# Optimization experiments

Measured on AMD Instinct MI355X. Metric: run time of the kernel, lower is better.

The kernel has to match this reference:

```python
import jax, jax.numpy as jnp
import numpy as np

VOCAB, D_MODEL, HEADS, PAD_ID = 32000, 512, 8, 0
D_K = D_MODEL // HEADS
EPS = 1e-5


def pos_encoding(T, d):
    pos = jnp.arange(T, dtype=jnp.float32)[:, None]              # [T,1]
    freqs = 1.0 / (10000.0 ** (jnp.arange(0, d, 2, dtype=jnp.float32) / d))
    ang = pos * freqs                                            # [T,d/2]
    pe = jnp.zeros((T, d), dtype=jnp.float32)
    pe = pe.at[:, 0::2].set(jnp.sin(ang)).at[:, 1::2].set(jnp.cos(ang))
    return pe


def layer_norm(x, g, b):
    mu = jnp.mean(x, axis=-1, keepdims=True)
    var = jnp.var(x, axis=-1, keepdims=True)
    return (x - mu) * jax.lax.rsqrt(var + EPS) * g + b


def setup_inputs() -> dict:
    key = jax.random.key(0)
    ks = jax.random.split(key, 12)
    B, T = 4, 2048
    s = 0.02
    inp = {
        "tokens": jax.random.randint(ks[0], (B, T), 0, VOCAB),
        "emb": jax.random.normal(ks[1], (VOCAB, D_MODEL), jnp.float32) * s,
        "wq": jax.random.normal(ks[2], (D_MODEL, D_MODEL), jnp.float32) * s,
        "bq": jnp.zeros((D_MODEL,), jnp.float32),
        "wk": jax.random.normal(ks[3], (D_MODEL, D_MODEL), jnp.float32) * s,
        "bk": jnp.zeros((D_MODEL,), jnp.float32),
        "wv": jax.random.normal(ks[4], (D_MODEL, D_MODEL), jnp.float32) * s,
        "bv": jnp.zeros((D_MODEL,), jnp.float32),
        "wo": jax.random.normal(ks[5], (D_MODEL, D_MODEL), jnp.float32) * s,
        "bo": jnp.zeros((D_MODEL,), jnp.float32),
        "w1": jax.random.normal(ks[6], (D_MODEL, 2 * D_MODEL), jnp.float32) * s,
        "b1": jnp.zeros((2 * D_MODEL,), jnp.float32),
        "w2": jax.random.normal(ks[7], (2 * D_MODEL, D_MODEL), jnp.float32) * s,
        "b2": jnp.zeros((D_MODEL,), jnp.float32),
        "ln1_g": jnp.ones((D_MODEL,), jnp.float32),
        "ln1_b": jnp.zeros((D_MODEL,), jnp.float32),
        "ln2_g": jnp.ones((D_MODEL,), jnp.float32),
        "ln2_b": jnp.zeros((D_MODEL,), jnp.float32),
    }
    return inp


def reference(tokens, emb, wq, bq, wk, bk, wv, bv, wo, bo,
              w1, b1, w2, b2, ln1_g, ln1_b, ln2_g, ln2_b):
    B, T = tokens.shape
    x = emb[tokens] * jnp.sqrt(jnp.float32(D_MODEL))             # [B,T,D]
    x = x + pos_encoding(T, D_MODEL)[None]                       # add PE
    q = (x @ wq + bq).reshape(B, T, HEADS, D_K)
    k = (x @ wk + bk).reshape(B, T, HEADS, D_K)
    v = (x @ wv + bv).reshape(B, T, HEADS, D_K)
    scores = jnp.einsum("bqhd,bkhd->bhqk", q, k) / jnp.sqrt(jnp.float32(D_K))
    key_pad_mask = tokens == PAD_ID                              # [B,T]
    neg = jnp.finfo(scores.dtype).min
    scores = jnp.where(key_pad_mask[:, None, None, :], neg, scores)
    attn = jax.nn.softmax(scores, axis=-1)                       # [B,H,T,T]
    av = jnp.einsum("bhqk,bkhd->bqhd", attn, v).reshape(B, T, D_MODEL)
    av = av @ wo + bo
    h = layer_norm(av + x, ln1_g, ln1_b)
    ff = jax.nn.relu(h @ w1 + b1) @ w2 + b2
    out = layer_norm(h + ff, ln2_g, ln2_b)
    return out, key_pad_mask
```

## Files before the change

kernel.cpp:

```cpp
#include <hip/hip_runtime.h>
#include <hip/hip_bf16.h>
#include <math.h>

#define D_MODEL 512
#define HEADS   8
#define D_K     64
#define T_SEQ   2048
#define B_SZ    4
#define NROWS   (B_SZ * T_SEQ)
#define KVB     64
#define KSPLIT  2
#define KHALF   (T_SEQ / KSPLIT)

#define BN 128
#define BKG 64

typedef __attribute__((ext_vector_type(8))) short short8;
typedef __attribute__((ext_vector_type(4))) float f32x4;
typedef __attribute__((ext_vector_type(4))) ushort bf16x4;
typedef __attribute__((ext_vector_type(4))) unsigned int u32x4;

typedef __attribute__((address_space(1))) const unsigned int as1_uint;
typedef __attribute__((address_space(3))) unsigned int as3_uint;

__device__ __forceinline__ ushort f2bf(float f) {
    union { float f; unsigned u; } v; v.f = f;
    unsigned u = v.u;
    unsigned r = (u + 0x7FFFu + ((u >> 16) & 1u)) >> 16;
    return (ushort)r;
}
__device__ __forceinline__ float bf2f(ushort u) {
    union { unsigned u; float f; } v; v.u = ((unsigned)u) << 16;
    return v.f;
}
__device__ __forceinline__ unsigned pk_bf16(float lo, float hi) {
    unsigned r;
    asm("v_cvt_pk_bf16_f32 %0, %1, %2" : "=v"(r) : "v"(lo), "v"(hi));
    return r;
}

__global__ __launch_bounds__(256) void k_prep(
    const int* __restrict__ tokens, const float* __restrict__ emb,
    const float* __restrict__ wq, const float* __restrict__ wk,
    const float* __restrict__ wv, const float* __restrict__ wo,
    const float* __restrict__ w1, const float* __restrict__ w2,
    const float* __restrict__ bq, const float* __restrict__ bk,
    const float* __restrict__ bv,
    ushort* __restrict__ xb, float* __restrict__ mask_out,
    ushort* __restrict__ wqkvT, ushort* __restrict__ woT,
    ushort* __restrict__ w1T, ushort* __restrict__ w2T,
    float* __restrict__ bqkv, float qsc)
{
    __shared__ ushort tls[32][33];
    int bid = blockIdx.x, tid = threadIdx.x;
    if (bid < 4096) {
        int row = bid * 2 + (tid >> 7);
        int t   = row & (T_SEQ - 1);
        int tok = tokens[row];
        int t2  = tid & 127;
        if (t2 == 0) mask_out[row] = (tok == 0) ? 1.0f : 0.0f;
        const float* e = emb + (size_t)tok * D_MODEL;
#pragma unroll
        for (int i = 0; i < 4; ++i) {
            int d = t2 + 128 * i;
            float freq = exp2f(-(float)(d & ~1) * 0.025952563240330564f);
            float sn, cs;
            sincosf((float)t * freq, &sn, &cs);
            float x = e[d] * 22.627416997969522f + ((d & 1) ? cs : sn);
            xb[(size_t)row * D_MODEL + d] = f2bf(x);
        }
        return;
    }
    const float* src; ushort* dst; float scale = 1.0f; int K, N, bx, by;
    if (bid < 5120) {
        int b = bid - 4096; int z = b >> 8; int rem = b & 255;
        bx = rem & 15; by = rem >> 4; K = 512; N = 512;
        src = (z == 0) ? wq : (z == 1) ? wk : (z == 2) ? wv : wo;
        dst = (z < 3) ? wqkvT + (size_t)z * 512 * 512 : woT;
        scale = (z == 0) ? qsc : 1.0f;
    } else if (bid < 5632) {
        int b = bid - 5120; bx = b & 31; by = b >> 5; K = 512; N = 1024; src = w1; dst = w1T;
    } else if (bid < 6144) {
        int b = bid - 5632; bx = b & 15; by = b >> 4; K = 1024; N = 512; src = w2; dst = w2T;
    } else {
        int i = (bid - 6144) * 256 + tid;
        if (i < 512)       bqkv[i] = bq[i] * qsc;
        else if (i < 1024) bqkv[i] = bk[i - 512];
        else if (i < 1536) bqkv[i] = bv[i - 1024];
        return;
    }
    int tx = tid & 31, ty = tid >> 5;
    int n0 = bx * 32, k0 = by * 32;
#pragma unroll
    for (int i = 0; i < 4; ++i)
        tls[ty + i * 8][tx] = f2bf(src[(size_t)(k0 + ty + i * 8) * N + n0 + tx] * scale);
    __syncthreads();
#pragma unroll
    for (int i = 0; i < 4; ++i)
        dst[(size_t)(n0 + ty + i * 8) * K + k0 + tx] = tls[tx][ty + i * 8];
}

template<int MODE, bool RELU, int BMT>
__global__ __launch_bounds__(256) void k_gemm_lds(
    const ushort* __restrict__ A, const ushort* __restrict__ BT,
    const float* __restrict__ bias, void* __restrict__ C0,
    void* __restrict__ C1, void* __restrict__ C2,
    int M, int N, int K)
{
    constexpr int MR = BMT / 32;
    __shared__ __attribute__((aligned(16))) ushort As[2][BMT * BKG];
    __shared__ __attribute__((aligned(16))) ushort Bs[2][BN * BKG];

    const int tid = threadIdx.x;
    const int w = tid >> 6, l = tid & 63;
    const int lr = l & 15, lg = l >> 4;
    const int wr = w >> 1, wc = w & 1;

    int bx = blockIdx.x, by = blockIdx.y;
    {
        int nx = gridDim.x, ny = gridDim.y;
        if ((ny & 7) == 0) {
            int lin = bx + nx * by;
            int xcd = lin & 7, idx = lin >> 3;
            int per = ny >> 3;
            by = xcd * per + (idx % per);
            bx = idx / per;
        }
    }
    const int brow0 = by * BMT;
    const int bcol0 = bx * BN;
    const int swz = lr & 15 & 7;

    f32x4 acc[MR][4] = {};
    const int nks = K >> 6;

#define STAGE(buf, k0)                                                          \
    {                                                                           \
        _Pragma("unroll")                                                       \
        for (int i = 0; i < BMT / 32; ++i) {                                    \
            int gi = w * (BMT * 2) + i * 64 + l;                                \
            int row = gi >> 3, slot = gi & 7;                                   \
            int g = slot ^ (row & 7);                                           \
            __builtin_amdgcn_global_load_lds(                                   \
                (as1_uint*)(A + (size_t)(brow0 + row) * K + (k0) + g * 8),      \
                (as3_uint*)(&As[buf][gi * 8]), 16, 0, 0);                       \
        }                                                                       \
        _Pragma("unroll")                                                       \
        for (int i = 0; i < 4; ++i) {                                           \
            int gi = w * 256 + i * 64 + l;                                      \
            int row = gi >> 3, slot = gi & 7;                                   \
            int g = slot ^ (row & 7);                                           \
            __builtin_amdgcn_global_load_lds(                                   \
                (as1_uint*)(BT + (size_t)(bcol0 + row) * K + (k0) + g * 8),     \
                (as3_uint*)(&Bs[buf][gi * 8]), 16, 0, 0);                       \
        }                                                                       \
    }

    STAGE(0, 0);
    __syncthreads();

    int buf = 0;
    for (int ks = 0; ks < nks; ++ks) {
        if (ks + 1 < nks) STAGE(buf ^ 1, (ks + 1) * BKG);
#pragma unroll
        for (int kk = 0; kk < 2; ++kk) {
            short8 af[MR], bfr[4];
#pragma unroll
            for (int m = 0; m < MR; ++m) {
                int row = wr * (BMT / 2) + m * 16 + lr;
                int slot = (kk * 4 + lg) ^ swz;
                af[m] = *(const short8*)(&As[buf][row * 64 + slot * 8]);
            }
#pragma unroll
            for (int n = 0; n < 4; ++n) {
                int row = wc * 64 + n * 16 + lr;
                int slot = (kk * 4 + lg) ^ swz;
                bfr[n] = *(const short8*)(&Bs[buf][row * 64 + slot * 8]);
            }
#pragma unroll
            for (int m = 0; m < MR; ++m)
#pragma unroll
                for (int n = 0; n < 4; ++n)
                    acc[m][n] = __builtin_amdgcn_mfma_f32_16x16x32_bf16(af[m], bfr[n], acc[m][n], 0, 0, 0);
        }
        __syncthreads();
        buf ^= 1;
    }
#undef STAGE

#pragma unroll
    for (int n = 0; n < 4; ++n) {
        int col = bcol0 + wc * 64 + n * 16 + lr;
        float bv = bias[col];
#pragma unroll
        for (int m = 0; m < MR; ++m) {
            int row0 = brow0 + wr * (BMT / 2) + m * 16 + 4 * lg;
            if constexpr (MODE == 2) {
                int seg = col >> 9, lc = col & 511;
                if (seg == 2) {
                    bf16x4 pk;
#pragma unroll
                    for (int j = 0; j < 4; ++j) pk[j] = f2bf(acc[m][n][j] + bv);
                    *(bf16x4*)((ushort*)C2 + (size_t)lc * M + row0) = pk;
                } else {
                    ushort* dst = (seg == 0) ? (ushort*)C0 : (ushort*)C1;
#pragma unroll
                    for (int j = 0; j < 4; ++j)
                        dst[(size_t)(row0 + j) * 512 + lc] = f2bf(acc[m][n][j] + bv);
                }
            } else if constexpr (MODE == 0) {
#pragma unroll
                for (int j = 0; j < 4; ++j) {
                    float v = acc[m][n][j] + bv;
                    if (RELU) v = fmaxf(v, 0.0f);
                    ((ushort*)C0)[(size_t)(row0 + j) * N + col] = f2bf(v);
                }
            } else {
#pragma unroll
                for (int j = 0; j < 4; ++j)
                    ((float*)C0)[(size_t)(row0 + j) * N + col] = acc[m][n][j] + bv;
            }
        }
    }
}

__global__ __launch_bounds__(512, 4) void k_attn(
    const ushort* __restrict__ Q, const ushort* __restrict__ Kb,
    const ushort* __restrict__ Vt, const int* __restrict__ tokens,
    ushort* __restrict__ O0, ushort* __restrict__ O1,
    float* __restrict__ lp)
{
    __shared__ __attribute__((aligned(16))) ushort Kl[2][KVB * 64];
    __shared__ __attribute__((aligned(16))) ushort Vl[2][KVB * 64];
    __shared__ __attribute__((aligned(16))) ushort Mbh[KHALF];
    __shared__ int padf[KHALF / KVB];

    const int tid = threadIdx.x;
    const int w = tid >> 6, l = tid & 63;
    const int lr = l & 15, lg = l >> 4;
    const int swz = lr & 7;

    int lin = blockIdx.x + 8 * (blockIdx.y + 8 * blockIdx.z);
    int xcd = lin & 7, idx = lin >> 3;
    int qt  = idx & 7;
    int grp = xcd + 8 * (idx >> 3);
    int ks  = grp & 1;
    int h   = (grp >> 1) & 7;
    int b   = grp >> 4;

    const int q0  = qt * 256 + w * 32;
    const int kb0 = ks * KHALF;

    const int gi   = w * 64 + l;
    const int srow = gi >> 3;
    const int sg   = gi & 7;
    const int sgx  = sg ^ (srow & 7);
    const ushort* Ksrc = Kb + ((size_t)(b * T_SEQ + kb0) + srow) * D_MODEL + h * D_K + sgx * 8;
    const int kbase = 32 * (sg >> 2) + 8 * ((sg >> 1) & 1) + 4 * (sg & 1);
    const ushort* Vsrc = Vt + (size_t)(h * D_K + srow) * NROWS + b * T_SEQ + kb0 + kbase;
    const int vds = srow * 128 + sgx * 16;

#define KSTAGE(bufi, kt_)                                                       \
    __builtin_amdgcn_global_load_lds(                                           \
        (as1_uint*)(Ksrc + (size_t)(kt_) * KVB * D_MODEL),                      \
        (as3_uint*)(&Kl[bufi][gi * 8]), 16, 0, 0);

    const ushort* Qh = Q + (size_t)b * T_SEQ * D_MODEL + h * D_K;
    short8 aq[2][2];
#pragma unroll
    for (int qs = 0; qs < 2; ++qs)
#pragma unroll
        for (int c2 = 0; c2 < 2; ++c2)
            aq[qs][c2] = *(const short8*)(Qh + (size_t)(q0 + qs * 16 + lr) * D_MODEL
                                          + c2 * 32 + 8 * lg);

    short8 vones;
#pragma unroll
    for (int i = 0; i < 8; ++i) vones[i] = (short)0x3F80;

    const int* tk = tokens + b * T_SEQ + kb0;
#pragma unroll
    for (int it = 0; it < KHALF / 512; ++it) {
        int i = tid + it * 512;
        bool pad = (tk[i] == 0);
        Mbh[i] = pad ? (ushort)0xFF7F : (ushort)0;
        unsigned long long bal = __ballot(pad);
        if (l == 0) padf[it * 8 + w] = (bal != 0ull);
    }

    f32x4 acc[2][4] = {};
    f32x4 acc_l[2] = {};

    {
        bf16x4 va = *(const bf16x4*)(Vsrc);
        bf16x4 vb2 = *(const bf16x4*)(Vsrc + 16);
        KSTAGE(0, 0);
        u32x4 pk = { ((const unsigned*)&va)[0], ((const unsigned*)&va)[1],
                     ((const unsigned*)&vb2)[0], ((const unsigned*)&vb2)[1] };
        *(u32x4*)((char*)Vl[0] + vds) = pk;
    }
    __syncthreads();

    int buf = 0;
    const int NT = KHALF / KVB;
    for (int kt = 0; kt < NT; ++kt) {
        bf16x4 vna, vnb;
        bool more = (kt + 1 < NT);
        if (more) {
            KSTAGE(buf ^ 1, kt + 1);
            vna = *(const bf16x4*)(Vsrc + (kt + 1) * KVB);
            vnb = *(const bf16x4*)(Vsrc + (kt + 1) * KVB + 16);
        }

        const ushort* Kt = Kl[buf];
        const ushort* Vb = Vl[buf];
        bool havePad = padf[kt];

        unsigned dw[2][4][2];
#pragma unroll
        for (int kh = 0; kh < 2; ++kh) {
            short8 kf[2][2];
#pragma unroll
            for (int i = 0; i < 2; ++i)
#pragma unroll
                for (int c2 = 0; c2 < 2; ++c2)
                    kf[i][c2] = *(const short8*)((const char*)Kt
                                + ((2 * kh + i) * 16 + lr) * 128
                                + (((c2 * 4 + lg) ^ swz) * 16));
#pragma unroll
            for (int qs = 0; qs < 2; ++qs)
#pragma unroll
                for (int i = 0; i < 2; ++i) {
                    int kb = 2 * kh + i;
                    __builtin_amdgcn_s_setprio(1);
                    f32x4 sf = {};
                    sf = __builtin_amdgcn_mfma_f32_16x16x32_bf16(kf[i][0], aq[qs][0], sf, 0, 0, 0);
                    sf = __builtin_amdgcn_mfma_f32_16x16x32_bf16(kf[i][1], aq[qs][1], sf, 0, 0, 0);
                    __builtin_amdgcn_s_setprio(0);
                    if (havePad) {
                        bf16x4 m4 = *(const bf16x4*)(Mbh + kt * KVB + kb * 16 + 4 * lg);
#pragma unroll
                        for (int j = 0; j < 4; ++j) sf[j] += bf2f(m4[j]);
                    }
                    dw[qs][kb][0] = pk_bf16(exp2f(sf[0]), exp2f(sf[1]));
                    dw[qs][kb][1] = pk_bf16(exp2f(sf[2]), exp2f(sf[3]));
                }
        }

#pragma unroll
        for (int ch = 0; ch < 2; ++ch) {
            short8 vf[2][2];
#pragma unroll
            for (int i = 0; i < 2; ++i)
#pragma unroll
                for (int kk = 0; kk < 2; ++kk)
                    vf[i][kk] = *(const short8*)((const char*)Vb
                                + ((2 * ch + i) * 16 + lr) * 128
                                + (((kk * 4 + lg) ^ swz) * 16));
            __builtin_amdgcn_s_setprio(1);
#pragma unroll
            for (int qs = 0; qs < 2; ++qs) {
                u32x4 pw0 = { dw[qs][0][0], dw[qs][0][1], dw[qs][1][0], dw[qs][1][1] };
                u32x4 pw1 = { dw[qs][2][0], dw[qs][2][1], dw[qs][3][0], dw[qs][3][1] };
                short8 pa0 = __builtin_bit_cast(short8, pw0);
                short8 pa1 = __builtin_bit_cast(short8, pw1);
#pragma unroll
                for (int i = 0; i < 2; ++i) {
                    int c = 2 * ch + i;
                    acc[qs][c] = __builtin_amdgcn_mfma_f32_16x16x32_bf16(vf[i][0], pa0, acc[qs][c], 0, 0, 0);
                    acc[qs][c] = __builtin_amdgcn_mfma_f32_16x16x32_bf16(vf[i][1], pa1, acc[qs][c], 0, 0, 0);
                }
                if (ch == 0) {
                    acc_l[qs] = __builtin_amdgcn_mfma_f32_16x16x32_bf16(vones, pa0, acc_l[qs], 0, 0, 0);
                    acc_l[qs] = __builtin_amdgcn_mfma_f32_16x16x32_bf16(vones, pa1, acc_l[qs], 0, 0, 0);
                }
            }
            __builtin_amdgcn_s_setprio(0);
        }

        if (more) {
            u32x4 pk = { ((const unsigned*)&vna)[0], ((const unsigned*)&vna)[1],
                         ((const unsigned*)&vnb)[0], ((const unsigned*)&vnb)[1] };
            *(u32x4*)((char*)Vl[buf ^ 1] + vds) = pk;
        }
        __syncthreads();
        buf ^= 1;
    }
#undef KSTAGE

    ushort* Op = (ks == 0) ? O0 : O1;
#pragma unroll
    for (int qs = 0; qs < 2; ++qs) {
        ushort* orow = Op + (size_t)(b * T_SEQ + q0 + qs * 16 + lr) * D_MODEL + h * D_K;
#pragma unroll
        for (int c = 0; c < 4; ++c) {
            bf16x4 pk;
#pragma unroll
            for (int j = 0; j < 4; ++j) pk[j] = f2bf(acc[qs][c][j]);
            *(bf16x4*)(orow + c * 16 + 4 * lg) = pk;
        }
        if (l < 16)
            lp[(size_t)(ks * 8 + h) * NROWS + b * T_SEQ + q0 + qs * 16 + l] = acc_l[qs][0];
    }
}

__global__ __launch_bounds__(256) void k_comb(
    ushort* __restrict__ O0, const ushort* __restrict__ O1,
    const float* __restrict__ lp)
{
    int g = blockIdx.x * 256 + threadIdx.x;
    int row = g >> 6, seg = g & 63;
    int h = seg >> 3;
    size_t off = (size_t)row * D_MODEL + seg * 8;
    short8 a = *(const short8*)(O0 + off);
    short8 c = *(const short8*)(O1 + off);
    float l0 = lp[(size_t)h * NROWS + row];
    float l1 = lp[(size_t)(8 + h) * NROWS + row];
    float rl = 1.0f / (l0 + l1);
    short8 r;
#pragma unroll
    for (int i = 0; i < 8; ++i)
        r[i] = (short)f2bf((bf2f((ushort)a[i]) + bf2f((ushort)c[i])) * rl);
    *(short8*)(O0 + off) = r;
}

template<bool A_BF16, bool RES_BF16, bool OUT_F32>
__global__ __launch_bounds__(256) void k_ln(
    const void* __restrict__ A, const void* __restrict__ Res,
    const float* __restrict__ g, const float* __restrict__ bb,
    float* __restrict__ of, ushort* __restrict__ ob)
{
    int row = blockIdx.x * 4 + (threadIdx.x >> 6);
    int l = threadIdx.x & 63;
    float v[8];
    float s = 0.0f, ss = 0.0f;
#pragma unroll
    for (int i = 0; i < 2; ++i) {
        int d0 = i * 256 + l * 4;
        f32x4 va, vb;
        if (A_BF16) {
            bf16x4 t = *(const bf16x4*)((const ushort*)A + (size_t)row * D_MODEL + d0);
#pragma unroll
            for (int j = 0; j < 4; ++j) va[j] = bf2f(t[j]);
        } else {
            va = *(const f32x4*)((const float*)A + (size_t)row * D_MODEL + d0);
        }
        if (RES_BF16) {
            bf16x4 t = *(const bf16x4*)((const ushort*)Res + (size_t)row * D_MODEL + d0);
#pragma unroll
            for (int j = 0; j < 4; ++j) vb[j] = bf2f(t[j]);
        } else {
            vb = *(const f32x4*)((const float*)Res + (size_t)row * D_MODEL + d0);
        }
#pragma unroll
        for (int j = 0; j < 4; ++j) {
            float x = va[j] + vb[j];
            v[i * 4 + j] = x; s += x; ss += x * x;
        }
    }
#pragma unroll
    for (int d = 1; d < 64; d <<= 1) { s += __shfl_xor(s, d); ss += __shfl_xor(ss, d); }
    float mu  = s * (1.0f / 512.0f);
    float var = ss * (1.0f / 512.0f) - mu * mu;
    float rs  = rsqrtf(var + 1e-5f);
#pragma unroll
    for (int i = 0; i < 2; ++i)
#pragma unroll
        for (int j = 0; j < 4; ++j) {
            int d = i * 256 + l * 4 + j;
            float o = (v[i * 4 + j] - mu) * rs * g[d] + bb[d];
            if (OUT_F32) of[(size_t)row * D_MODEL + d] = o;
            else         ob[(size_t)row * D_MODEL + d] = f2bf(o);
        }
}

extern "C" void kernel_launch(void* const* d_in, const int* in_sizes, int n_in,
                              void* d_out, int out_size, void* d_ws, size_t ws_size,
                              hipStream_t stream)
{
    const int*   tokens = (const int*)  d_in[0];
    const float* emb    = (const float*)d_in[1];
    const float* wq     = (const float*)d_in[2];
    const float* bq     = (const float*)d_in[3];
    const float* wk     = (const float*)d_in[4];
    const float* bk     = (const float*)d_in[5];
    const float* wv     = (const float*)d_in[6];
    const float* bv     = (const float*)d_in[7];
    const float* wo     = (const float*)d_in[8];
    const float* bo     = (const float*)d_in[9];
    const float* w1     = (const float*)d_in[10];
    const float* b1     = (const float*)d_in[11];
    const float* w2     = (const float*)d_in[12];
    const float* b2     = (const float*)d_in[13];
    const float* ln1_g  = (const float*)d_in[14];
    const float* ln1_b  = (const float*)d_in[15];
    const float* ln2_g  = (const float*)d_in[16];
    const float* ln2_b  = (const float*)d_in[17];

    char* ws = (char*)d_ws;
    ushort* xb   = (ushort*)(ws + 0);
    ushort* Qb   = (ushort*)(ws + 8388608);
    ushort* Kbuf = (ushort*)(ws + 16777216);
    ushort* Vt   = (ushort*)(ws + 25165824);
    ushort* atb  = (ushort*)(ws + 33554432);
    ushort* AVb  = (ushort*)(ws + 41943040);
    ushort* wqkvT = (ushort*)(ws + 50331648);
    ushort* woT  = wqkvT + 1536 * 512;
    ushort* w1T  = woT + 262144;
    ushort* w2T  = w1T + 524288;
    float*  bqkv = (float*)(w2T + 524288);
    float*  lpart = bqkv + 2048;

    ushort* hb   = Qb;
    ushort* ff1b = Kbuf;
    ushort* ff2b = AVb;

    float* out_f    = (float*)d_out;
    float* mask_out = out_f + (size_t)NROWS * D_MODEL;

    const float QSC = 0.18033688011112042f;

    k_prep<<<6150, 256, 0, stream>>>(
        tokens, emb, wq, wk, wv, wo, w1, w2, bq, bk, bv,
        xb, mask_out, wqkvT, woT, w1T, w2T, bqkv, QSC);

    k_gemm_lds<2, false, 128><<<dim3(12, 64), 256, 0, stream>>>(
        xb, wqkvT, bqkv, Qb, Kbuf, Vt, NROWS, 1536, 512);

    k_attn<<<dim3(8, 8, 8), 512, 0, stream>>>(
        Qb, Kbuf, Vt, tokens, atb, AVb, lpart);
    k_comb<<<2048, 256, 0, stream>>>(atb, AVb, lpart);

    k_gemm_lds<0, false, 64><<<dim3(4, 128), 256, 0, stream>>>(
        atb, woT, bo, AVb, nullptr, nullptr, NROWS, 512, 512);

    k_ln<true, true, false><<<NROWS / 4, 256, 0, stream>>>(
        AVb, xb, ln1_g, ln1_b, nullptr, hb);

    k_gemm_lds<0, true, 64><<<dim3(8, 128), 256, 0, stream>>>(
        hb, w1T, b1, ff1b, nullptr, nullptr, NROWS, 1024, 512);
    k_gemm_lds<0, false, 64><<<dim3(4, 128), 256, 0, stream>>>(
        ff1b, w2T, b2, ff2b, nullptr, nullptr, NROWS, 512, 1024);

    k_ln<true, true, true><<<NROWS / 4, 256, 0, stream>>>(
        ff2b, hb, ln2_g, ln2_b, out_f, nullptr);
}
```

Before: 156.5 us.

## Fuse split-K attention combine into output-projection GEMM A-tile staging

Removes the separate combine kernel that merged the two key-split attention partial outputs. The Wo GEMM now loads both partial outputs per A tile, adds them, scales by a precomputed reciprocal normalizer from a tiny new kernel, and writes bf16 to LDS. This saves a full read-modify-write pass over the attention output, but the A path switches from async global-to-LDS DMA to register loads plus math. Buffers are also reassigned to avoid aliasing, and the attention key loop gets an unroll-2 pragma.

```diff
diff --git a/kernel.cpp b/kernel.cpp
--- a/kernel.cpp
+++ b/kernel.cpp
@@ -100,9 +100,17 @@
         dst[(size_t)(n0 + ty + i * 8) * K + k0 + tx] = tls[tx][ty + i * 8];
 }
 
-template<int MODE, bool RELU, int BMT>
+__global__ __launch_bounds__(256) void k_rl(const float* __restrict__ lp,
+                                            float* __restrict__ rl) {
+    int i = blockIdx.x * 256 + threadIdx.x;
+    rl[i] = 1.0f / (lp[i] + lp[8 * NROWS + i]);
+}
+
+template<int MODE, bool RELU, int BMT, bool COMBA>
 __global__ __launch_bounds__(256) void k_gemm_lds(
-    const ushort* __restrict__ A, const ushort* __restrict__ BT,
+    const ushort* __restrict__ A, const ushort* __restrict__ A2,
+    const float* __restrict__ rlb,
+    const ushort* __restrict__ BT,
     const float* __restrict__ bias, void* __restrict__ C0,
     void* __restrict__ C1, void* __restrict__ C2,
     int M, int N, int K)
@@ -129,12 +137,24 @@
     }
     const int brow0 = by * BMT;
     const int bcol0 = bx * BN;
-    const int swz = lr & 15 & 7;
+    const int swz = lr & 7;
 
     f32x4 acc[MR][4] = {};
     const int nks = K >> 6;
 
-#define STAGE(buf, k0)                                                          \
+#define STAGE_B(buf, k0)                                                        \
+    {                                                                           \
+        _Pragma("unroll")                                                       \
+        for (int i = 0; i < 4; ++i) {                                           \
+            int gi = w * 256 + i * 64 + l;                                      \
+            int row = gi >> 3, slot = gi & 7;                                   \
+            int g = slot ^ (row & 7);                                           \
+            __builtin_amdgcn_global_load_lds(                                   \
+                (as1_uint*)(BT + (size_t)(bcol0 + row) * K + (k0) + g * 8),     \
+                (as3_uint*)(&Bs[buf][gi * 8]), 16, 0, 0);                       \
+        }                                                                       \
+    }
+#define STAGE_A_DMA(buf, k0)                                                    \
     {                                                                           \
         _Pragma("unroll")                                                       \
         for (int i = 0; i < BMT / 32; ++i) {                                    \
@@ -145,15 +165,38 @@
                 (as1_uint*)(A + (size_t)(brow0 + row) * K + (k0) + g * 8),      \
                 (as3_uint*)(&As[buf][gi * 8]), 16, 0, 0);                       \
         }                                                                       \
+    }
+#define STAGE_A_COMB(buf, k0)                                                   \
+    {                                                                           \
+        int head = (k0) >> 6;                                                   \
         _Pragma("unroll")                                                       \
-        for (int i = 0; i < 4; ++i) {                                           \
-            int gi = w * 256 + i * 64 + l;                                      \
+        for (int i = 0; i < BMT / 32; ++i) {                                    \
+            int gi = w * (BMT * 2) + i * 64 + l;                                \
             int row = gi >> 3, slot = gi & 7;                                   \
             int g = slot ^ (row & 7);                                           \
-            __builtin_amdgcn_global_load_lds(                                   \
-                (as1_uint*)(BT + (size_t)(bcol0 + row) * K + (k0) + g * 8),     \
-                (as3_uint*)(&Bs[buf][gi * 8]), 16, 0, 0);                       \
+            size_t off = (size_t)(brow0 + row) * K + (k0) + g * 8;              \
+            bf16x4 a0 = *(const bf16x4*)(A + off);                              \
+            bf16x4 a1 = *(const bf16x4*)(A + off + 4);                          \
+            bf16x4 c0 = *(const bf16x4*)(A2 + off);                             \
+            bf16x4 c1 = *(const bf16x4*)(A2 + off + 4);                         \
+            float r = rlb[(size_t)head * NROWS + brow0 + row];                  \
+            u32x4 pk;                                                           \
+            pk[0] = pk_bf16((bf2f(a0[0]) + bf2f(c0[0])) * r,                    \
+                            (bf2f(a0[1]) + bf2f(c0[1])) * r);                   \
+            pk[1] = pk_bf16((bf2f(a0[2]) + bf2f(c0[2])) * r,                    \
+                            (bf2f(a0[3]) + bf2f(c0[3])) * r);                   \
+            pk[2] = pk_bf16((bf2f(a1[0]) + bf2f(c1[0])) * r,                    \
+                            (bf2f(a1[1]) + bf2f(c1[1])) * r);                   \
+            pk[3] = pk_bf16((bf2f(a1[2]) + bf2f(c1[2])) * r,                    \
+                            (bf2f(a1[3]) + bf2f(c1[3])) * r);                   \
+            *(u32x4*)(&As[buf][gi * 8]) = pk;                                   \
         }                                                                       \
+    }
+#define STAGE(buf, k0)                                                          \
+    {                                                                           \
+        if constexpr (COMBA) { STAGE_A_COMB(buf, k0); }                         \
+        else                 { STAGE_A_DMA(buf, k0); }                          \
+        STAGE_B(buf, k0);                                                       \
     }
 
     STAGE(0, 0);
@@ -187,6 +230,9 @@
         buf ^= 1;
     }
 #undef STAGE
+#undef STAGE_A_COMB
+#undef STAGE_A_DMA
+#undef STAGE_B
 
 #pragma unroll
     for (int n = 0; n < 4; ++n) {
@@ -303,6 +349,7 @@
 
     int buf = 0;
     const int NT = KHALF / KVB;
+#pragma unroll 2
     for (int kt = 0; kt < NT; ++kt) {
         bf16x4 vna, vnb;
         bool more = (kt + 1 < NT);
@@ -402,26 +449,6 @@
         if (l < 16)
             lp[(size_t)(ks * 8 + h) * NROWS + b * T_SEQ + q0 + qs * 16 + l] = acc_l[qs][0];
     }
-}
-
-__global__ __launch_bounds__(256) void k_comb(
-    ushort* __restrict__ O0, const ushort* __restrict__ O1,
-    const float* __restrict__ lp)
-{
-    int g = blockIdx.x * 256 + threadIdx.x;
-    int row = g >> 6, seg = g & 63;
-    int h = seg >> 3;
-    size_t off = (size_t)row * D_MODEL + seg * 8;
-    short8 a = *(const short8*)(O0 + off);
-    short8 c = *(const short8*)(O1 + off);
-    float l0 = lp[(size_t)h * NROWS + row];
-    float l1 = lp[(size_t)(8 + h) * NROWS + row];
-    float rl = 1.0f / (l0 + l1);
-    short8 r;
-#pragma unroll
-    for (int i = 0; i < 8; ++i)
-        r[i] = (short)f2bf((bf2f((ushort)a[i]) + bf2f((ushort)c[i])) * rl);
-    *(short8*)(O0 + off) = r;
 }
 
 template<bool A_BF16, bool RES_BF16, bool OUT_F32>
@@ -510,10 +537,14 @@
     ushort* w2T  = w1T + 524288;
     float*  bqkv = (float*)(w2T + 524288);
     float*  lpart = bqkv + 2048;
+    float*  rlbuf = lpart + 2 * 8 * NROWS;
+    float*  WOf   = (float*)(rlbuf + 8 * NROWS);
 
     ushort* hb   = Qb;
     ushort* ff1b = Kbuf;
     ushort* ff2b = AVb;
+    ushort* wob  = AVb;
+    (void)WOf;
 
     float* out_f    = (float*)d_out;
     float* mask_out = out_f + (size_t)NROWS * D_MODEL;
@@ -524,24 +555,24 @@
         tokens, emb, wq, wk, wv, wo, w1, w2, bq, bk, bv,
         xb, mask_out, wqkvT, woT, w1T, w2T, bqkv, QSC);
 
-    k_gemm_lds<2, false, 128><<<dim3(12, 64), 256, 0, stream>>>(
-        xb, wqkvT, bqkv, Qb, Kbuf, Vt, NROWS, 1536, 512);
+    k_gemm_lds<2, false, 128, false><<<dim3(12, 64), 256, 0, stream>>>(
+        xb, nullptr, nullptr, wqkvT, bqkv, Qb, Kbuf, Vt, NROWS, 1536, 512);
 
     k_attn<<<dim3(8, 8, 8), 512, 0, stream>>>(
         Qb, Kbuf, Vt, tokens, atb, AVb, lpart);
-    k_comb<<<2048, 256, 0, stream>>>(atb, AVb, lpart);
-
-    k_gemm_lds<0, false, 64><<<dim3(4, 128), 256, 0, stream>>>(
-        atb, woT, bo, AVb, nullptr, nullptr, NROWS, 512, 512);
+    k_rl<<<8 * NROWS / 256, 256, 0, stream>>>(lpart, rlbuf);
+
+    k_gemm_lds<0, false, 64, true><<<dim3(4, 128), 256, 0, stream>>>(
+        atb, AVb, rlbuf, woT, bo, Qb, nullptr, nullptr, NROWS, 512, 512);
 
     k_ln<true, true, false><<<NROWS / 4, 256, 0, stream>>>(
-        AVb, xb, ln1_g, ln1_b, nullptr, hb);
-
-    k_gemm_lds<0, true, 64><<<dim3(8, 128), 256, 0, stream>>>(
-        hb, w1T, b1, ff1b, nullptr, nullptr, NROWS, 1024, 512);
-    k_gemm_lds<0, false, 64><<<dim3(4, 128), 256, 0, stream>>>(
-        ff1b, w2T, b2, ff2b, nullptr, nullptr, NROWS, 512, 1024);
+        Qb, xb, ln1_g, ln1_b, nullptr, atb);
+
+    k_gemm_lds<0, true, 64, false><<<dim3(8, 128), 256, 0, stream>>>(
+        atb, nullptr, nullptr, w1T, b1, ff1b, nullptr, nullptr, NROWS, 1024, 512);
+    k_gemm_lds<0, false, 64, false><<<dim3(4, 128), 256, 0, stream>>>(
+        ff1b, nullptr, nullptr, w2T, b2, ff2b, nullptr, nullptr, NROWS, 512, 1024);
 
     k_ln<true, true, true><<<NROWS / 4, 256, 0, stream>>>(
-        ff2b, hb, ln2_g, ln2_b, out_f, nullptr);
-}
+        ff2b, atb, ln2_g, ln2_b, out_f, nullptr);
+}
```

Result: faster. 150.4 us (-3.9%).
